# Kernel tuning notes

Measured on AMD Instinct MI355X. Metric: run time of the kernel, lower is better.

Reference implementation:

```python
import jax, jax.numpy as jnp
import numpy as np

B, L, D, H, DH, MAX_SEQ = 2, 2048, 512, 8, 64, 2048


def setup_inputs() -> dict:
    key = jax.random.key(0)
    ks = jax.random.split(key, 9)
    w = 0.02
    return {
        "q": jax.random.normal(ks[0], (B, L, D), jnp.float32),
        "k": jax.random.normal(ks[1], (B, L, D), jnp.float32),
        "v": jax.random.normal(ks[2], (B, L, D), jnp.float32),
        "Wq_w": jax.random.normal(ks[3], (D, D), jnp.float32) * w,
        "Wq_b": jnp.zeros((D,), jnp.float32),
        "Wk_w": jax.random.normal(ks[4], (D, D), jnp.float32) * w,
        "Wk_b": jnp.zeros((D,), jnp.float32),
        "Wv_w": jax.random.normal(ks[5], (D, D), jnp.float32) * w,
        "Wv_b": jnp.zeros((D,), jnp.float32),
        "fc_w": jax.random.normal(ks[6], (D, D), jnp.float32) * w,
        "fc_b": jnp.zeros((D,), jnp.float32),
        "E": jax.random.normal(ks[7], (MAX_SEQ, DH), jnp.float32),
        "mask": jnp.triu(jnp.ones((L, L), jnp.int32), k=1)[None, None],  # 1 = masked
    }


def reference(q, k, v, Wq_w, Wq_b, Wk_w, Wk_b, Wv_w, Wv_b, fc_w, fc_b, E, mask):
    b, lq, d = q.shape

    def proj(x, w, bias):
        # torch Linear: x @ W.T + b, then split heads -> [b, h, l, dh]
        y = x @ w.T + bias
        return y.reshape(b, -1, H, DH).transpose(0, 2, 1, 3)

    qh, kh, vh = proj(q, Wq_w, Wq_b), proj(k, Wk_w, Wk_b), proj(v, Wv_w, Wv_b)
    len_q, len_k = qh.shape[2], kh.shape[2]

    # relative embedding slice (starting_point = max(0, max_seq - len_q))
    e = E[max(0, MAX_SEQ - len_q):, :]          # [m, dh], m == len_q here
    m = e.shape[0]

    QE = jnp.einsum('bhld,md->bhlm', qh, e)      # [b,h,lq,m]
    # qe_masking: keep column j of row i iff j >= m-1-i
    keep = (jnp.arange(m)[None, :] >= (m - 1 - jnp.arange(len_q))[:, None])
    QE = QE * keep.astype(QE.dtype)

    # skewing: left-pad last dim, reshape swapping trailing dims, drop first row
    padded = jnp.pad(QE, ((0, 0), (0, 0), (0, 0), (1, 0)))      # [b,h,lq,m+1]
    Srel = padded.reshape(b, H, m + 1, len_q)[:, :, 1:, :]       # [b,h,m,lq]
    if len_k > len_q:
        Srel = jnp.pad(Srel, ((0, 0), (0, 0), (0, len_k - len_q), (0, 0)))
    elif len_k < len_q:
        Srel = Srel[:, :, :, :len_k]

    QKt = jnp.einsum('bhld,bhmd->bhlm', qh, kh)                  # [b,h,lq,lk]
    logits = (QKt + Srel) / jnp.sqrt(jnp.float32(DH))
    logits = logits + mask.astype(logits.dtype) * jnp.float32(-1e9)
    attn = jax.nn.softmax(logits, axis=-1)
    out = jnp.einsum('bhlm,bhmd->bhld', attn, vh)                # [b,h,lq,dh]
    out = out.transpose(0, 2, 1, 3).reshape(b, len_q, d)
    out = out @ fc_w.T + fc_b
    return out, attn
```

## Files before the change

### kernel.cpp

```cpp
#include <hip/hip_runtime.h>
#include <hip/hip_bf16.h>
#include <cstdint>

typedef __bf16 bf16;
typedef __attribute__((ext_vector_type(8))) __bf16 bf16x8;
typedef __attribute__((ext_vector_type(4))) __bf16 bf16x4;
typedef __attribute__((ext_vector_type(4))) float f32x4;

#define MFMA16 __builtin_amdgcn_mfma_f32_16x16x32_bf16
#define MASKV (-1e30f)

static constexpr int Lq  = 2048;
static constexpr int BKt = 64;

__device__ __forceinline__ void async_load16(const void* g, void* l) {
  __builtin_amdgcn_global_load_lds(
      (__attribute__((address_space(1))) void*)g,
      (__attribute__((address_space(3))) void*)l, 16, 0, 0);
}

__global__ void convert_all(const float* __restrict__ q, const float* __restrict__ k,
                            const float* __restrict__ v, const float* __restrict__ wq,
                            const float* __restrict__ wk, const float* __restrict__ wv,
                            const float* __restrict__ fc, const float* __restrict__ E,
                            bf16* q_bf, bf16* k_bf, bf16* v_bf, bf16* wq_bf,
                            bf16* wk_bf, bf16* wv_bf, bf16* fc_bf, bf16* E_bf,
                            float* s_buf)
{
  int i = blockIdx.x * blockDim.x + threadIdx.x;
  const float* src; bf16* dst; int rel;
  if      (i < 524288)  { src = q;  dst = q_bf;  rel = i; }
  else if (i < 1048576) { src = k;  dst = k_bf;  rel = i - 524288; }
  else if (i < 1572864) { src = v;  dst = v_bf;  rel = i - 1048576; }
  else if (i < 1638400) { src = wq; dst = wq_bf; rel = i - 1572864; }
  else if (i < 1703936) { src = wk; dst = wk_bf; rel = i - 1638400; }
  else if (i < 1769472) { src = wv; dst = wv_bf; rel = i - 1703936; }
  else if (i < 1835008) { src = fc; dst = fc_bf; rel = i - 1769472; }
  else if (i < 1867776) { src = E;  dst = E_bf;  rel = i - 1835008; }
  else if (i < 1875968) {
    ((float4*)s_buf)[i - 1867776] = make_float4(0.f, 0.f, 0.f, 0.f);
    return;
  }
  else return;
  float4 x = *(const float4*)(src + (size_t)rel * 4);
  bf16x4 o;
  o[0] = (bf16)x.x; o[1] = (bf16)x.y; o[2] = (bf16)x.z; o[3] = (bf16)x.w;
  *(bf16x4*)(dst + (size_t)rel * 4) = o;
}

template<int MODE>
__device__ __forceinline__
void gemm512_core(const bf16* __restrict__ A, const bf16* __restrict__ Bm,
                  const float* __restrict__ bias, void* __restrict__ Cv,
                  int tm, int tn, char* lA, char* lB)
{
  const int tid = threadIdx.x, lane = tid & 63, wv = tid >> 6;
  const int wr = wv >> 1, wc = wv & 1;

  f32x4 acc[4][4];
#pragma unroll
  for (int m = 0; m < 4; ++m)
#pragma unroll
    for (int n = 0; n < 4; ++n) acc[m][n] = (f32x4){0.f, 0.f, 0.f, 0.f};

  for (int k0 = 0; k0 < 512; k0 += 64) {
    __syncthreads();
#pragma unroll
    for (int it = 0; it < 4; ++it) {
      int slot = it * 256 + wv * 64 + lane;
      int row = slot >> 3, c = slot & 7;
      int gk = k0 + ((c ^ (row & 7)) * 8);
      async_load16(A  + (size_t)(tm * 128 + row) * 512 + gk, lA + (it * 256 + wv * 64) * 16);
      async_load16(Bm + (size_t)(tn * 128 + row) * 512 + gk, lB + (it * 256 + wv * 64) * 16);
    }
    __syncthreads();
#pragma unroll
    for (int kc = 0; kc < 2; ++kc) {
      bf16x8 af[4], bfr[4];
#pragma unroll
      for (int m = 0; m < 4; ++m) {
        int row = wr * 64 + m * 16 + (lane & 15);
        int ch = ((lane >> 4) + kc * 4) ^ (row & 7);
        af[m] = *(const bf16x8*)(lA + row * 128 + ch * 16);
      }
#pragma unroll
      for (int n = 0; n < 4; ++n) {
        int row = wc * 64 + n * 16 + (lane & 15);
        int ch = ((lane >> 4) + kc * 4) ^ (row & 7);
        bfr[n] = *(const bf16x8*)(lB + row * 128 + ch * 16);
      }
#pragma unroll
      for (int m = 0; m < 4; ++m)
#pragma unroll
        for (int n = 0; n < 4; ++n)
          acc[m][n] = MFMA16(af[m], bfr[n], acc[m][n], 0, 0, 0);
    }
  }

#pragma unroll
  for (int m = 0; m < 4; ++m)
#pragma unroll
    for (int n = 0; n < 4; ++n)
#pragma unroll
      for (int r = 0; r < 4; ++r) {
        int gi = tm * 128 + wr * 64 + m * 16 + 4 * (lane >> 4) + r;
        int gj = tn * 128 + wc * 64 + n * 16 + (lane & 15);
        float vv = acc[m][n][r] + ((MODE == 2) ? bias[gi] : bias[gj]);
        if (MODE == 3) {
          ((float*)Cv)[(size_t)gi * 512 + gj] = vv;
        } else if (MODE == 2) {
          int h = gi >> 6, dh = gi & 63, b = gj >> 11, l = gj & 2047;
          ((bf16*)Cv)[((size_t)((b * 8 + h) * 64 + dh)) * 2048 + l] = (bf16)vv;
        } else {
          int b = gi >> 11, l = gi & 2047, h = gj >> 6, dh = gj & 63;
          ((bf16*)Cv)[((size_t)((b * 8 + h) * 2048 + l)) * 64 + dh] = (bf16)vv;
        }
      }
}

__global__ __launch_bounds__(256, 2)
void gemm_qkv(const bf16* __restrict__ q_bf, const bf16* __restrict__ k_bf,
              const bf16* __restrict__ v_bf, const bf16* __restrict__ wq_bf,
              const bf16* __restrict__ wk_bf, const bf16* __restrict__ wv_bf,
              const float* __restrict__ wq_b, const float* __restrict__ wk_b,
              const float* __restrict__ wv_b,
              bf16* __restrict__ qh, bf16* __restrict__ kh, bf16* __restrict__ vt)
{
  __shared__ __align__(16) char lA[16384];
  __shared__ __align__(16) char lB[16384];
  const int z = blockIdx.z;
  if (z == 0)      gemm512_core<0>(q_bf, wq_bf, wq_b, qh, blockIdx.x, blockIdx.y, lA, lB);
  else if (z == 1) gemm512_core<0>(k_bf, wk_bf, wk_b, kh, blockIdx.x, blockIdx.y, lA, lB);
  else             gemm512_core<2>(wv_bf, v_bf, wv_b, vt, blockIdx.y, blockIdx.x, lA, lB);
}

__global__ __launch_bounds__(256, 2)
void gemm_fc(const bf16* __restrict__ A, const bf16* __restrict__ Bm,
             const float* __restrict__ bias, float* __restrict__ Cv)
{
  __shared__ __align__(16) char lA[16384];
  __shared__ __align__(16) char lB[16384];
  gemm512_core<3>(A, Bm, bias, Cv, blockIdx.x, blockIdx.y, lA, lB);
}

__device__ __forceinline__ void stage_k(const bf16* __restrict__ kb, int j0,
                                        char* dst, int tid) {
#pragma unroll
  for (int it = 0; it < 2; ++it) {
    int slot = it * 256 + tid;
    int row = slot >> 3, c = slot & 7;
    async_load16(kb + (size_t)(j0 + row) * 64 + ((c ^ (row & 7)) * 8), dst + slot * 16);
  }
}
__device__ __forceinline__ void stage_v(const bf16* __restrict__ vb, int j0,
                                        char* dst, int tid) {
#pragma unroll
  for (int it = 0; it < 2; ++it) {
    int slot = it * 256 + tid;
    int row = slot >> 3, c = slot & 7;
    async_load16(vb + (size_t)row * Lq + j0 + ((c ^ (row & 7)) * 8), dst + slot * 16);
  }
}

__device__ __forceinline__ void attn_logits_sh(
    int i0, int j0, int wvx, int lane,
    const bf16x8 qf0, const bf16x8 qf1,
    const bf16* __restrict__ Ebf, const char* lk, f32x4 acc_s[4])
{
  const int rbase = i0 + wvx * 16 - j0 - 63;
  f32x4 acc_t[5];
#pragma unroll
  for (int cf = 0; cf < 5; ++cf) {
    int r = rbase + cf * 16 + (lane & 15);
    int re = 2047 - r; re = re < 0 ? 0 : (re > 2047 ? 2047 : re);
    const bf16* ep = Ebf + (size_t)re * 64 + (lane >> 4) * 8;
    f32x4 a = (f32x4){0.f, 0.f, 0.f, 0.f};
    a = MFMA16(qf0, *(const bf16x8*)ep, a, 0, 0, 0);
    a = MFMA16(qf1, *(const bf16x8*)(ep + 32), a, 0, 0, 0);
    acc_t[cf] = a;
  }
#pragma unroll
  for (int cf = 0; cf < 4; ++cf) {
    int key = cf * 16 + (lane & 15);
    int c0 = (lane >> 4) ^ (key & 7);
    int c1 = ((lane >> 4) + 4) ^ (key & 7);
    f32x4 a = (f32x4){0.f, 0.f, 0.f, 0.f};
    a = MFMA16(qf0, *(const bf16x8*)(lk + key * 128 + c0 * 16), a, 0, 0, 0);
    a = MFMA16(qf1, *(const bf16x8*)(lk + key * 128 + c1 * 16), a, 0, 0, 0);
    acc_s[cf] = a;
  }
  const int g = lane >> 4, b = lane & 15;
#pragma unroll
  for (int r = 0; r < 4; ++r) {
    const int qw  = 4 * g + r;
    const int sl  = (lane & 48) | ((63 + qw - b) & 15);
    const bool hi = qw > b;
#pragma unroll
    for (int cf = 0; cf < 4; ++cf) {
      float vhi = __shfl(acc_t[4 - cf][r], sl);
      float vlo = __shfl(acc_t[3 - cf][r], sl);
      float t = hi ? vhi : vlo;
      float vv = (acc_s[cf][r] + t) * 0.125f;
      if (j0 + cf * 16 + b > i0 + wvx * 16 + qw) vv = MASKV;
      acc_s[cf][r] = vv;
    }
  }
}

__global__ __launch_bounds__(256, 2)
void produce(const bf16* __restrict__ qh, const bf16* __restrict__ kh,
             const bf16* __restrict__ vt, const bf16* __restrict__ Ebf,
             bf16* __restrict__ P_scr, float* __restrict__ O_slots,
             float* __restrict__ s_buf, float* __restrict__ attn_out)
{
  __shared__ __align__(16) char lds_k[4][64 * 128];
  __shared__ __align__(16) char lds_v[4][64 * 128];
  __shared__ __align__(16) char lds_p[4][16 * 64 * 2];

  const int tid = threadIdx.x, lane = tid & 63, wvx = tid >> 6;
  const int n    = blockIdx.x;
  const int xcd  = n & 7;
  const int r0   = n >> 3;
  const int bh   = 2 * xcd + (r0 & 1);
  const int u    = r0 >> 1;
  const int f    = u & 7;
  const int qt   = 31 - (u >> 3);
  const int nc   = (qt >> 2) + 1;
  if (f >= nc) return;
  const int i0   = qt * 64;
  const int jbeg = f * 4;
  const int jend = (jbeg + 4 < qt + 1) ? jbeg + 4 : qt + 1;
  const int nt   = jend - jbeg;

  const bf16* qb = qh + (size_t)bh * Lq * 64;
  const bf16* kb = kh + (size_t)bh * Lq * 64;
  const bf16* vb = vt + (size_t)bh * 64 * Lq;
  float* attn_b = attn_out + (size_t)bh * Lq * Lq;
  bf16* P_b = P_scr + (size_t)bh * Lq * Lq;
  bf16* pst = (bf16*)lds_p[wvx];

  for (int t = 0; t < nt; ++t) {
    stage_k(kb, (jbeg + t) * BKt, lds_k[t], tid);
    stage_v(vb, (jbeg + t) * BKt, lds_v[t], tid);
  }

  const int qrow = i0 + wvx * 16 + (lane & 15);
  const bf16x8 qf0 = *(const bf16x8*)(qb + (size_t)qrow * 64 + (lane >> 4) * 8);
  const bf16x8 qf1 = *(const bf16x8*)(qb + (size_t)qrow * 64 + 32 + (lane >> 4) * 8);

  f32x4 acc_s[4];
  f32x4 acc_o[4];
  float s_acc[4] = {0.f, 0.f, 0.f, 0.f};
#pragma unroll
  for (int nn = 0; nn < 4; ++nn) acc_o[nn] = (f32x4){0.f, 0.f, 0.f, 0.f};

  asm volatile("s_waitcnt vmcnt(0)" ::: "memory");
  __builtin_amdgcn_s_barrier();

  for (int t = 0; t < nt; ++t) {
    const int j0 = (jbeg + t) * BKt;
    attn_logits_sh(i0, j0, wvx, lane, qf0, qf1, Ebf, lds_k[t], acc_s);
#pragma unroll
    for (int cf = 0; cf < 4; ++cf) {
      int kl = cf * 16 + (lane & 15);
      int chs = kl >> 3;
#pragma unroll
      for (int r = 0; r < 4; ++r) {
        int qw = 4 * (lane >> 4) + r;
        float p = __expf(acc_s[cf][r]);
        s_acc[r] += p;
        pst[qw * 64 + ((chs ^ (qw & 7)) * 8) + (kl & 7)] = (bf16)p;
      }
    }
    asm volatile("s_waitcnt lgkmcnt(0)" ::: "memory");
    __builtin_amdgcn_sched_barrier(0);
#pragma unroll
    for (int it = 0; it < 2; ++it) {
      int qw = it * 8 + (lane >> 3);
      int c = lane & 7;
      bf16x8 pv = *(const bf16x8*)(pst + qw * 64 + ((c ^ (qw & 7)) * 8));
      *(bf16x8*)(P_b + (size_t)(i0 + wvx * 16 + qw) * Lq + j0 + c * 8) = pv;
    }
    __builtin_amdgcn_s_setprio(1);
#pragma unroll
    for (int kc = 0; kc < 2; ++kc) {
      int qa = lane & 15;
      int cha = (kc * 4 + (lane >> 4)) ^ (qa & 7);
      bf16x8 pf = *(const bf16x8*)(pst + qa * 64 + cha * 8);
#pragma unroll
      for (int nn = 0; nn < 4; ++nn) {
        int dh = nn * 16 + (lane & 15);
        int chv = (kc * 4 + (lane >> 4)) ^ (dh & 7);
        bf16x8 vf = *(const bf16x8*)(lds_v[t] + dh * 128 + chv * 16);
        acc_o[nn] = MFMA16(pf, vf, acc_o[nn], 0, 0, 0);
      }
    }
    __builtin_amdgcn_s_setprio(0);
  }

  float* oslot = O_slots + (size_t)(((bh * 32 + qt) * 8 + f)) * 4096;
#pragma unroll
  for (int nn = 0; nn < 4; ++nn)
#pragma unroll
    for (int r = 0; r < 4; ++r) {
      int row = wvx * 16 + 4 * (lane >> 4) + r;
      oslot[row * 64 + nn * 16 + (lane & 15)] = acc_o[nn][r];
    }

#pragma unroll
  for (int r = 0; r < 4; ++r) {
    float s = s_acc[r];
    for (int d = 1; d < 16; d <<= 1) s += __shfl_xor(s, d);
    if ((lane & 15) == 0)
      atomicAdd(&s_buf[bh * Lq + i0 + wvx * 16 + 4 * (lane >> 4) + r], s);
  }

  for (int jz = qt + 1 + f; jz < 32; jz += nc) {
    const int j0 = jz * BKt;
#pragma unroll
    for (int kk = 0; kk < 4; ++kk) {
      int idx = kk * 256 + tid;
      int row = idx >> 4, c4 = idx & 15;
      float* p = attn_b + (size_t)(i0 + row) * Lq + j0 + c4 * 4;
      *(float4*)p = make_float4(0.f, 0.f, 0.f, 0.f);
    }
  }
}

__global__ __launch_bounds__(256, 8)
void finish(const bf16* __restrict__ P_scr, const float* __restrict__ s_buf,
            float* __restrict__ attn_out)
{
  const int lane = threadIdx.x & 63, wvx = threadIdx.x >> 6;
  const int row = blockIdx.x * 4 + wvx;
  const int i   = row & 2047;
  const int ncols = (i & ~63) + 64;
  const float inv = 1.f / s_buf[row];
  const bf16* src = P_scr + (size_t)row * Lq;
  float* dst = attn_out + (size_t)row * Lq;
  for (int c = lane * 4; c < ncols; c += 256) {
    bf16x4 pv = *(const bf16x4*)(src + c);
    float4 fo;
    fo.x = (float)pv[0] * inv;
    fo.y = (float)pv[1] * inv;
    fo.z = (float)pv[2] * inv;
    fo.w = (float)pv[3] * inv;
    *(float4*)(dst + c) = fo;
  }
}

__global__ void combine_o(const float* __restrict__ O_slots,
                          const float* __restrict__ s_buf, bf16* __restrict__ oh)
{
  const int sid = blockIdx.x;
  const int bh = sid >> 5, qt = sid & 31;
  const int nch = (qt >> 2) + 1;
  const float* base = O_slots + (size_t)(bh * 32 + qt) * 8 * 4096;
  const int b = bh >> 3, h = bh & 7;
  for (int e4 = threadIdx.x; e4 < 1024; e4 += 256) {
    float4 s = make_float4(0.f, 0.f, 0.f, 0.f);
    for (int ff = 0; ff < nch; ++ff) {
      float4 x = *(const float4*)(base + ff * 4096 + e4 * 4);
      s.x += x.x; s.y += x.y; s.z += x.z; s.w += x.w;
    }
    int row = e4 >> 4;
    int col = (e4 & 15) * 4;
    int ig = qt * 64 + row;
    float inv = 1.f / s_buf[bh * Lq + ig];
    bf16x4 o;
    o[0] = (bf16)(s.x * inv); o[1] = (bf16)(s.y * inv);
    o[2] = (bf16)(s.z * inv); o[3] = (bf16)(s.w * inv);
    *(bf16x4*)(oh + (size_t)(b * 2048 + ig) * 512 + h * 64 + col) = o;
  }
}

extern "C" void kernel_launch(void* const* d_in, const int* in_sizes, int n_in,
                              void* d_out, int out_size, void* d_ws, size_t ws_size,
                              hipStream_t stream) {
  const float* q    = (const float*)d_in[0];
  const float* k    = (const float*)d_in[1];
  const float* v    = (const float*)d_in[2];
  const float* wq   = (const float*)d_in[3];
  const float* wq_b = (const float*)d_in[4];
  const float* wk   = (const float*)d_in[5];
  const float* wk_b = (const float*)d_in[6];
  const float* wv   = (const float*)d_in[7];
  const float* wv_b = (const float*)d_in[8];
  const float* fc   = (const float*)d_in[9];
  const float* fc_b = (const float*)d_in[10];
  const float* E    = (const float*)d_in[11];

  if (ws_size < 233177088) return;
  char* ws = (char*)d_ws;
  bf16*  q_bf    = (bf16*)(ws);
  bf16*  k_bf    = (bf16*)(ws + 4194304);
  bf16*  v_bf    = (bf16*)(ws + 8388608);
  bf16*  wq_bf   = (bf16*)(ws + 12582912);
  bf16*  wk_bf   = (bf16*)(ws + 13107200);
  bf16*  wv_bf   = (bf16*)(ws + 13631488);
  bf16*  fc_bf   = (bf16*)(ws + 14155776);
  bf16*  E_bf    = (bf16*)(ws + 14680064);
  float* s_buf   = (float*)(ws + 14942208);
  bf16*  qh_bf   = (bf16*)(ws + 15073280);
  bf16*  kh_bf   = (bf16*)(ws + 19267584);
  bf16*  vt_bf   = (bf16*)(ws + 23461888);
  bf16*  oh_bf   = (bf16*)(ws + 27656192);
  float* O_slots = (float*)(ws + 31850496);
  bf16*  P_scr   = (bf16*)(ws + 98959360);

  float* out_f  = (float*)d_out;
  float* attn_f = out_f + 2097152;

  convert_all<<<7328, 256, 0, stream>>>(q, k, v, wq, wk, wv, fc, E,
      q_bf, k_bf, v_bf, wq_bf, wk_bf, wv_bf, fc_bf, E_bf, s_buf);
  gemm_qkv<<<dim3(32, 4, 3), 256, 0, stream>>>(q_bf, k_bf, v_bf,
      wq_bf, wk_bf, wv_bf, wq_b, wk_b, wv_b, qh_bf, kh_bf, vt_bf);
  produce<<<4096, 256, 0, stream>>>(qh_bf, kh_bf, vt_bf, E_bf,
                                    P_scr, O_slots, s_buf, attn_f);
  finish<<<8192, 256, 0, stream>>>(P_scr, s_buf, attn_f);
  combine_o<<<512, 256, 0, stream>>>(O_slots, s_buf, oh_bf);
  gemm_fc<<<dim3(32, 4), 256, 0, stream>>>(oh_bf, fc_bf, fc_b, out_f);
}
```

Before: 196.8 us.

## Precompute Q·E relative-position table via GEMM and restructure P storage and finish

Adds a gemm_T kernel that materializes the full Q·E^T relative table per head (lower triangle of tiles) in bf16. The produce kernel then reads skewed values from it instead of doing extra MFMAs and shuffles, computes S^T with swapped MFMA operands, and reads V straight from global memory rather than staging it in LDS. P is written in a permuted register-native layout, and finish transposes it through LDS while also zero-filling the masked region. Combine_o goes through an LDS transpose. The intent is to cut MFMA and shuffle work in the hot kernel, at the cost of a large extra write and read of the T table and a bigger workspace.

```diff
diff --git a/kernel.cpp b/kernel.cpp
--- a/kernel.cpp
+++ b/kernel.cpp
@@ -17,6 +17,14 @@
   __builtin_amdgcn_global_load_lds(
       (__attribute__((address_space(1))) void*)g,
       (__attribute__((address_space(3))) void*)l, 16, 0, 0);
+}
+
+__device__ __forceinline__ unsigned pack2bf(float lo, float hi) {
+  bf16 a = (bf16)lo, c = (bf16)hi;
+  unsigned short ua, uc;
+  __builtin_memcpy(&ua, &a, 2);
+  __builtin_memcpy(&uc, &c, 2);
+  return ((unsigned)uc << 16) | ua;
 }
 
 __global__ void convert_all(const float* __restrict__ q, const float* __restrict__ k,
@@ -143,6 +151,74 @@
   gemm512_core<3>(A, Bm, bias, Cv, blockIdx.x, blockIdx.y, lA, lB);
 }
 
+__global__ __launch_bounds__(256, 2)
+void gemm_T(const bf16* __restrict__ qh, const bf16* __restrict__ E_bf,
+            bf16* __restrict__ T_full)
+{
+  __shared__ __align__(16) char lA[16384];
+  __shared__ __align__(16) char lB[16384];
+  const int tid = threadIdx.x, lane = tid & 63, wv = tid >> 6;
+  const int wr = wv >> 1, wc = wv & 1;
+  const int bh = blockIdx.y;
+  int x = blockIdx.x, ti = 0;
+  while (x > ti) { x -= ti + 1; ++ti; }
+  const int td = x;
+  const bf16* A = qh + (size_t)bh * Lq * 64;
+  bf16* Tb = T_full + (size_t)bh * Lq * 2048;
+
+#pragma unroll
+  for (int it = 0; it < 4; ++it) {
+    int slot = it * 256 + wv * 64 + lane;
+    int row = slot >> 3, c = slot & 7;
+    int gk = (c ^ (row & 7)) * 8;
+    async_load16(A + (size_t)(ti * 128 + row) * 64 + gk, lA + (it * 256 + wv * 64) * 16);
+    async_load16(E_bf + (size_t)(2047 - td * 128 - row) * 64 + gk,
+                 lB + (it * 256 + wv * 64) * 16);
+  }
+
+  f32x4 acc[4][4];
+#pragma unroll
+  for (int m = 0; m < 4; ++m)
+#pragma unroll
+    for (int n = 0; n < 4; ++n) acc[m][n] = (f32x4){0.f, 0.f, 0.f, 0.f};
+
+  asm volatile("s_waitcnt vmcnt(0)" ::: "memory");
+  __builtin_amdgcn_s_barrier();
+
+#pragma unroll
+  for (int kc = 0; kc < 2; ++kc) {
+    bf16x8 af[4], bfr[4];
+#pragma unroll
+    for (int m = 0; m < 4; ++m) {
+      int row = wr * 64 + m * 16 + (lane & 15);
+      int ch = ((lane >> 4) + kc * 4) ^ (row & 7);
+      af[m] = *(const bf16x8*)(lA + row * 128 + ch * 16);
+    }
+#pragma unroll
+    for (int n = 0; n < 4; ++n) {
+      int row = wc * 64 + n * 16 + (lane & 15);
+      int ch = ((lane >> 4) + kc * 4) ^ (row & 7);
+      bfr[n] = *(const bf16x8*)(lB + row * 128 + ch * 16);
+    }
+#pragma unroll
+    for (int m = 0; m < 4; ++m)
+#pragma unroll
+      for (int n = 0; n < 4; ++n)
+        acc[m][n] = MFMA16(af[m], bfr[n], acc[m][n], 0, 0, 0);
+  }
+
+#pragma unroll
+  for (int m = 0; m < 4; ++m)
+#pragma unroll
+    for (int n = 0; n < 4; ++n)
+#pragma unroll
+      for (int r = 0; r < 4; ++r) {
+        int gi = ti * 128 + wr * 64 + m * 16 + 4 * (lane >> 4) + r;
+        int gj = td * 128 + wc * 64 + n * 16 + (lane & 15);
+        Tb[(size_t)gi * 2048 + gj] = (bf16)acc[m][n][r];
+      }
+}
+
 __device__ __forceinline__ void stage_k(const bf16* __restrict__ kb, int j0,
                                         char* dst, int tid) {
 #pragma unroll
@@ -152,80 +228,26 @@
     async_load16(kb + (size_t)(j0 + row) * 64 + ((c ^ (row & 7)) * 8), dst + slot * 16);
   }
 }
-__device__ __forceinline__ void stage_v(const bf16* __restrict__ vb, int j0,
-                                        char* dst, int tid) {
-#pragma unroll
-  for (int it = 0; it < 2; ++it) {
-    int slot = it * 256 + tid;
-    int row = slot >> 3, c = slot & 7;
-    async_load16(vb + (size_t)row * Lq + j0 + ((c ^ (row & 7)) * 8), dst + slot * 16);
-  }
-}
-
-__device__ __forceinline__ void attn_logits_sh(
-    int i0, int j0, int wvx, int lane,
-    const bf16x8 qf0, const bf16x8 qf1,
-    const bf16* __restrict__ Ebf, const char* lk, f32x4 acc_s[4])
-{
-  const int rbase = i0 + wvx * 16 - j0 - 63;
-  f32x4 acc_t[5];
-#pragma unroll
-  for (int cf = 0; cf < 5; ++cf) {
-    int r = rbase + cf * 16 + (lane & 15);
-    int re = 2047 - r; re = re < 0 ? 0 : (re > 2047 ? 2047 : re);
-    const bf16* ep = Ebf + (size_t)re * 64 + (lane >> 4) * 8;
-    f32x4 a = (f32x4){0.f, 0.f, 0.f, 0.f};
-    a = MFMA16(qf0, *(const bf16x8*)ep, a, 0, 0, 0);
-    a = MFMA16(qf1, *(const bf16x8*)(ep + 32), a, 0, 0, 0);
-    acc_t[cf] = a;
-  }
-#pragma unroll
-  for (int cf = 0; cf < 4; ++cf) {
-    int key = cf * 16 + (lane & 15);
-    int c0 = (lane >> 4) ^ (key & 7);
-    int c1 = ((lane >> 4) + 4) ^ (key & 7);
-    f32x4 a = (f32x4){0.f, 0.f, 0.f, 0.f};
-    a = MFMA16(qf0, *(const bf16x8*)(lk + key * 128 + c0 * 16), a, 0, 0, 0);
-    a = MFMA16(qf1, *(const bf16x8*)(lk + key * 128 + c1 * 16), a, 0, 0, 0);
-    acc_s[cf] = a;
-  }
-  const int g = lane >> 4, b = lane & 15;
-#pragma unroll
-  for (int r = 0; r < 4; ++r) {
-    const int qw  = 4 * g + r;
-    const int sl  = (lane & 48) | ((63 + qw - b) & 15);
-    const bool hi = qw > b;
-#pragma unroll
-    for (int cf = 0; cf < 4; ++cf) {
-      float vhi = __shfl(acc_t[4 - cf][r], sl);
-      float vlo = __shfl(acc_t[3 - cf][r], sl);
-      float t = hi ? vhi : vlo;
-      float vv = (acc_s[cf][r] + t) * 0.125f;
-      if (j0 + cf * 16 + b > i0 + wvx * 16 + qw) vv = MASKV;
-      acc_s[cf][r] = vv;
-    }
-  }
-}
 
 __global__ __launch_bounds__(256, 2)
 void produce(const bf16* __restrict__ qh, const bf16* __restrict__ kh,
-             const bf16* __restrict__ vt, const bf16* __restrict__ Ebf,
-             bf16* __restrict__ P_scr, float* __restrict__ O_slots,
-             float* __restrict__ s_buf, float* __restrict__ attn_out)
+             const bf16* __restrict__ vt, const bf16* __restrict__ Tf,
+             unsigned* __restrict__ P_perm, float* __restrict__ O_slots,
+             float* __restrict__ s_buf)
 {
   __shared__ __align__(16) char lds_k[4][64 * 128];
-  __shared__ __align__(16) char lds_v[4][64 * 128];
-  __shared__ __align__(16) char lds_p[4][16 * 64 * 2];
-
-  const int tid = threadIdx.x, lane = tid & 63, wvx = tid >> 6;
-  const int n    = blockIdx.x;
-  const int xcd  = n & 7;
-  const int r0   = n >> 3;
-  const int bh   = 2 * xcd + (r0 & 1);
-  const int u    = r0 >> 1;
-  const int f    = u & 7;
-  const int qt   = 31 - (u >> 3);
-  const int nc   = (qt >> 2) + 1;
+  __shared__ __align__(16) unsigned strip_l[4][16 * 36];
+
+  const int tid = threadIdx.x, lane = tid & 63;
+  const int wvx = tid >> 6, b = lane & 15, g = lane >> 4;
+  const int n   = blockIdx.x;
+  const int xcd = n & 7;
+  const int r0  = n >> 3;
+  const int bh  = 2 * xcd + (r0 & 1);
+  const int u   = r0 >> 1;
+  const int f   = u & 7;
+  const int qt  = 31 - (u >> 3);
+  const int nc  = (qt >> 2) + 1;
   if (f >= nc) return;
   const int i0   = qt * 64;
   const int jbeg = f * 4;
@@ -235,142 +257,168 @@
   const bf16* qb = qh + (size_t)bh * Lq * 64;
   const bf16* kb = kh + (size_t)bh * Lq * 64;
   const bf16* vb = vt + (size_t)bh * 64 * Lq;
-  float* attn_b = attn_out + (size_t)bh * Lq * Lq;
-  bf16* P_b = P_scr + (size_t)bh * Lq * Lq;
-  bf16* pst = (bf16*)lds_p[wvx];
-
-  for (int t = 0; t < nt; ++t) {
+  const bf16* Tb = Tf + (size_t)bh * Lq * 2048;
+
+  for (int t = 0; t < nt; ++t)
     stage_k(kb, (jbeg + t) * BKt, lds_k[t], tid);
-    stage_v(vb, (jbeg + t) * BKt, lds_v[t], tid);
-  }
-
-  const int qrow = i0 + wvx * 16 + (lane & 15);
-  const bf16x8 qf0 = *(const bf16x8*)(qb + (size_t)qrow * 64 + (lane >> 4) * 8);
-  const bf16x8 qf1 = *(const bf16x8*)(qb + (size_t)qrow * 64 + 32 + (lane >> 4) * 8);
-
-  f32x4 acc_s[4];
+
+  const int qrow = i0 + wvx * 16 + b;
+  const bf16x8 qf0 = *(const bf16x8*)(qb + (size_t)qrow * 64 + g * 8);
+  const bf16x8 qf1 = *(const bf16x8*)(qb + (size_t)qrow * 64 + 32 + g * 8);
+  const bf16* trow = Tb + (size_t)qrow * 2048;
+
+  unsigned* sw = strip_l[wvx];
   f32x4 acc_o[4];
-  float s_acc[4] = {0.f, 0.f, 0.f, 0.f};
 #pragma unroll
   for (int nn = 0; nn < 4; ++nn) acc_o[nn] = (f32x4){0.f, 0.f, 0.f, 0.f};
+  float s_lane = 0.f;
 
   asm volatile("s_waitcnt vmcnt(0)" ::: "memory");
   __builtin_amdgcn_s_barrier();
 
   for (int t = 0; t < nt; ++t) {
-    const int j0 = (jbeg + t) * BKt;
-    attn_logits_sh(i0, j0, wvx, lane, qf0, qf1, Ebf, lds_k[t], acc_s);
+    const int jt = jbeg + t;
+    const int j0 = jt * BKt;
+    const bf16* tp = trow + (qrow - j0 - 4 * g);
+    float tv[4][4];
+#pragma unroll
+    for (int cf = 0; cf < 4; ++cf)
+#pragma unroll
+      for (int r = 0; r < 4; ++r)
+        tv[cf][r] = (float)tp[-(16 * cf + r)];
+
+    unsigned pk[4][2];
 #pragma unroll
     for (int cf = 0; cf < 4; ++cf) {
-      int kl = cf * 16 + (lane & 15);
-      int chs = kl >> 3;
+      const int key = 16 * cf + b;
+      const int c0 = g ^ (key & 7), c1 = (g + 4) ^ (key & 7);
+      f32x4 a = (f32x4){0.f, 0.f, 0.f, 0.f};
+      a = MFMA16(*(const bf16x8*)(lds_k[t] + key * 128 + c0 * 16), qf0, a, 0, 0, 0);
+      a = MFMA16(*(const bf16x8*)(lds_k[t] + key * 128 + c1 * 16), qf1, a, 0, 0, 0);
+      float p[4];
 #pragma unroll
       for (int r = 0; r < 4; ++r) {
-        int qw = 4 * (lane >> 4) + r;
-        float p = __expf(acc_s[cf][r]);
-        s_acc[r] += p;
-        pst[qw * 64 + ((chs ^ (qw & 7)) * 8) + (kl & 7)] = (bf16)p;
-      }
-    }
+        const int kgl = j0 + 16 * cf + 4 * g + r;
+        float vv = (a[r] + tv[cf][r]) * 0.125f;
+        if (kgl > qrow) vv = MASKV;
+        p[r] = __expf(vv);
+        s_lane += p[r];
+      }
+      pk[cf][0] = pack2bf(p[0], p[1]);
+      pk[cf][1] = pack2bf(p[2], p[3]);
+    }
+    unsigned* Pp = P_perm +
+        ((size_t)(bh * 128 + (i0 >> 4) + wvx) * 32 + jt) * 512;
+#pragma unroll
+    for (int cf = 0; cf < 4; ++cf)
+#pragma unroll
+      for (int s = 0; s < 2; ++s) {
+        Pp[(2 * cf + s) * 64 + lane] = pk[cf][s];
+        sw[b * 36 + 8 * cf + 2 * g + s] = pk[cf][s];
+      }
     asm volatile("s_waitcnt lgkmcnt(0)" ::: "memory");
     __builtin_amdgcn_sched_barrier(0);
-#pragma unroll
-    for (int it = 0; it < 2; ++it) {
-      int qw = it * 8 + (lane >> 3);
-      int c = lane & 7;
-      bf16x8 pv = *(const bf16x8*)(pst + qw * 64 + ((c ^ (qw & 7)) * 8));
-      *(bf16x8*)(P_b + (size_t)(i0 + wvx * 16 + qw) * Lq + j0 + c * 8) = pv;
-    }
     __builtin_amdgcn_s_setprio(1);
 #pragma unroll
     for (int kc = 0; kc < 2; ++kc) {
-      int qa = lane & 15;
-      int cha = (kc * 4 + (lane >> 4)) ^ (qa & 7);
-      bf16x8 pf = *(const bf16x8*)(pst + qa * 64 + cha * 8);
+      const bf16x8 pB = *(const bf16x8*)&sw[b * 36 + 16 * kc + 4 * g];
 #pragma unroll
       for (int nn = 0; nn < 4; ++nn) {
-        int dh = nn * 16 + (lane & 15);
-        int chv = (kc * 4 + (lane >> 4)) ^ (dh & 7);
-        bf16x8 vf = *(const bf16x8*)(lds_v[t] + dh * 128 + chv * 16);
-        acc_o[nn] = MFMA16(pf, vf, acc_o[nn], 0, 0, 0);
+        const int dh = 16 * nn + b;
+        const bf16* vp = vb + (size_t)dh * Lq + j0 + kc * 32 + g * 8;
+        acc_o[nn] = MFMA16(*(const bf16x8*)vp, pB, acc_o[nn], 0, 0, 0);
       }
     }
     __builtin_amdgcn_s_setprio(0);
   }
 
-  float* oslot = O_slots + (size_t)(((bh * 32 + qt) * 8 + f)) * 4096;
+  float* oslot = O_slots + (size_t)((bh * 32 + qt) * 8 + f) * 4096;
 #pragma unroll
   for (int nn = 0; nn < 4; ++nn)
 #pragma unroll
-    for (int r = 0; r < 4; ++r) {
-      int row = wvx * 16 + 4 * (lane >> 4) + r;
-      oslot[row * 64 + nn * 16 + (lane & 15)] = acc_o[nn][r];
-    }
-
-#pragma unroll
-  for (int r = 0; r < 4; ++r) {
-    float s = s_acc[r];
-    for (int d = 1; d < 16; d <<= 1) s += __shfl_xor(s, d);
-    if ((lane & 15) == 0)
-      atomicAdd(&s_buf[bh * Lq + i0 + wvx * 16 + 4 * (lane >> 4) + r], s);
-  }
-
-  for (int jz = qt + 1 + f; jz < 32; jz += nc) {
-    const int j0 = jz * BKt;
-#pragma unroll
-    for (int kk = 0; kk < 4; ++kk) {
-      int idx = kk * 256 + tid;
-      int row = idx >> 4, c4 = idx & 15;
-      float* p = attn_b + (size_t)(i0 + row) * Lq + j0 + c4 * 4;
-      *(float4*)p = make_float4(0.f, 0.f, 0.f, 0.f);
-    }
-  }
+    for (int r = 0; r < 4; ++r)
+      oslot[(16 * nn + 4 * g + r) * 64 + wvx * 16 + b] = acc_o[nn][r];
+
+  float s = s_lane;
+  s += __shfl_xor(s, 16);
+  s += __shfl_xor(s, 32);
+  if (lane < 16) atomicAdd(&s_buf[bh * Lq + i0 + wvx * 16 + b], s);
 }
 
 __global__ __launch_bounds__(256, 8)
-void finish(const bf16* __restrict__ P_scr, const float* __restrict__ s_buf,
+void finish(const unsigned* __restrict__ P_perm, const float* __restrict__ s_buf,
             float* __restrict__ attn_out)
 {
-  const int lane = threadIdx.x & 63, wvx = threadIdx.x >> 6;
-  const int row = blockIdx.x * 4 + wvx;
-  const int i   = row & 2047;
-  const int ncols = (i & ~63) + 64;
-  const float inv = 1.f / s_buf[row];
-  const bf16* src = P_scr + (size_t)row * Lq;
-  float* dst = attn_out + (size_t)row * Lq;
-  for (int c = lane * 4; c < ncols; c += 256) {
-    bf16x4 pv = *(const bf16x4*)(src + c);
-    float4 fo;
-    fo.x = (float)pv[0] * inv;
-    fo.y = (float)pv[1] * inv;
-    fo.z = (float)pv[2] * inv;
-    fo.w = (float)pv[3] * inv;
-    *(float4*)(dst + c) = fo;
-  }
-}
-
-__global__ void combine_o(const float* __restrict__ O_slots,
-                          const float* __restrict__ s_buf, bf16* __restrict__ oh)
-{
-  const int sid = blockIdx.x;
+  __shared__ unsigned lt[16][36];
+  const int tid = threadIdx.x, lane = tid & 63, wvx = tid >> 6;
+  const int strip = blockIdx.x;
+  const int bh = strip >> 7, sl = strip & 127;
+  float* attn_b = attn_out + (size_t)bh * Lq * Lq + (size_t)(sl * 16) * Lq;
+  const unsigned* Pp = P_perm + (size_t)strip * 32 * 512;
+  const int jt_max = sl >> 2;
+  const int half = lane >> 5, l32 = lane & 31;
+  const float inv0 = 1.f / s_buf[bh * Lq + sl * 16 + wvx * 4 + half];
+  const float inv1 = 1.f / s_buf[bh * Lq + sl * 16 + wvx * 4 + half + 2];
+  const int w0 = tid >> 6, l0 = tid & 63;
+  const int d0c = 8 * (w0 >> 1) + 2 * (l0 >> 4) + (w0 & 1);
+  const int w1 = (tid + 256) >> 6;
+  const int d1c = 8 * (w1 >> 1) + 2 * (l0 >> 4) + (w1 & 1);
+  const int drow = l0 & 15;
+
+  for (int jt = 0; jt < 32; ++jt) {
+    if (jt <= jt_max) {
+      unsigned a = Pp[jt * 512 + tid];
+      unsigned c = Pp[jt * 512 + tid + 256];
+      __syncthreads();
+      lt[drow][d0c] = a;
+      lt[drow][d1c] = c;
+      __syncthreads();
+#pragma unroll
+      for (int p = 0; p < 2; ++p) {
+        int row = wvx * 4 + p * 2 + half;
+        unsigned uu = lt[row][l32];
+        float inv = p ? inv1 : inv0;
+        float2 o;
+        o.x = __uint_as_float(uu << 16) * inv;
+        o.y = __uint_as_float(uu & 0xffff0000u) * inv;
+        *(float2*)(attn_b + (size_t)row * Lq + jt * 64 + l32 * 2) = o;
+      }
+    } else {
+#pragma unroll
+      for (int p = 0; p < 2; ++p) {
+        int row = wvx * 4 + p * 2 + half;
+        *(float2*)(attn_b + (size_t)row * Lq + jt * 64 + l32 * 2) =
+            make_float2(0.f, 0.f);
+      }
+    }
+  }
+}
+
+__global__ __launch_bounds__(256, 4)
+void combine_o(const float* __restrict__ O_slots, const float* __restrict__ s_buf,
+               bf16* __restrict__ oh)
+{
+  __shared__ float lt[64 * 65];
+  const int sid = blockIdx.x, t = threadIdx.x;
   const int bh = sid >> 5, qt = sid & 31;
   const int nch = (qt >> 2) + 1;
-  const float* base = O_slots + (size_t)(bh * 32 + qt) * 8 * 4096;
+  const float* base = O_slots + (size_t)sid * 8 * 4096;
+#pragma unroll 1
+  for (int i = 0; i < 16; ++i) {
+    int e = t + 256 * i;
+    float s = 0.f;
+    for (int ff = 0; ff < nch; ++ff) s += base[ff * 4096 + e];
+    lt[(e & 63) * 65 + (e >> 6)] = s;
+  }
+  __syncthreads();
   const int b = bh >> 3, h = bh & 7;
-  for (int e4 = threadIdx.x; e4 < 1024; e4 += 256) {
-    float4 s = make_float4(0.f, 0.f, 0.f, 0.f);
-    for (int ff = 0; ff < nch; ++ff) {
-      float4 x = *(const float4*)(base + ff * 4096 + e4 * 4);
-      s.x += x.x; s.y += x.y; s.z += x.z; s.w += x.w;
-    }
-    int row = e4 >> 4;
-    int col = (e4 & 15) * 4;
-    int ig = qt * 64 + row;
-    float inv = 1.f / s_buf[bh * Lq + ig];
-    bf16x4 o;
-    o[0] = (bf16)(s.x * inv); o[1] = (bf16)(s.y * inv);
-    o[2] = (bf16)(s.z * inv); o[3] = (bf16)(s.w * inv);
-    *(bf16x4*)(oh + (size_t)(b * 2048 + ig) * 512 + h * 64 + col) = o;
+#pragma unroll 1
+  for (int i = 0; i < 16; ++i) {
+    int o = t + 256 * i;
+    int row = o >> 6, dh = o & 63;
+    float inv = 1.f / s_buf[bh * Lq + qt * 64 + row];
+    oh[(size_t)(b * 2048 + qt * 64 + row) * 512 + h * 64 + dh] =
+        (bf16)(lt[row * 65 + dh] * inv);
   }
 }
 
@@ -390,7 +438,7 @@
   const float* fc_b = (const float*)d_in[10];
   const float* E    = (const float*)d_in[11];
 
-  if (ws_size < 233177088) return;
+  if (ws_size < 367394816) return;
   char* ws = (char*)d_ws;
   bf16*  q_bf    = (bf16*)(ws);
   bf16*  k_bf    = (bf16*)(ws + 4194304);
@@ -406,7 +454,8 @@
   bf16*  vt_bf   = (bf16*)(ws + 23461888);
   bf16*  oh_bf   = (bf16*)(ws + 27656192);
   float* O_slots = (float*)(ws + 31850496);
-  bf16*  P_scr   = (bf16*)(ws + 98959360);
+  unsigned* P_perm = (unsigned*)(ws + 98959360);
+  bf16*  T_full  = (bf16*)(ws + 233177088);
 
   float* out_f  = (float*)d_out;
   float* attn_f = out_f + 2097152;
@@ -415,9 +464,10 @@
       q_bf, k_bf, v_bf, wq_bf, wk_bf, wv_bf, fc_bf, E_bf, s_buf);
   gemm_qkv<<<dim3(32, 4, 3), 256, 0, stream>>>(q_bf, k_bf, v_bf,
       wq_bf, wk_bf, wv_bf, wq_b, wk_b, wv_b, qh_bf, kh_bf, vt_bf);
-  produce<<<4096, 256, 0, stream>>>(qh_bf, kh_bf, vt_bf, E_bf,
-                                    P_scr, O_slots, s_buf, attn_f);
-  finish<<<8192, 256, 0, stream>>>(P_scr, s_buf, attn_f);
+  gemm_T<<<dim3(136, 16), 256, 0, stream>>>(qh_bf, E_bf, T_full);
+  produce<<<4096, 256, 0, stream>>>(qh_bf, kh_bf, vt_bf, T_full,
+                                    P_perm, O_slots, s_buf);
+  finish<<<2048, 256, 0, stream>>>(P_perm, s_buf, attn_f);
   combine_o<<<512, 256, 0, stream>>>(O_slots, s_buf, oh_bf);
   gemm_fc<<<dim3(32, 4), 256, 0, stream>>>(oh_bf, fc_bf, fc_b, out_f);
 }
```

Measured after the change: 297.0 us. 50.9% more time.
